# Kernel optimization log

Measured on AMD Instinct MI355X. Metric: run time of the kernel, lower is better.

The kernel has to match this reference:

```python
import jax, jax.numpy as jnp
import numpy as np

HIDDEN = 50
EPS = 1e-5


def setup_inputs() -> dict:
    key = jax.random.key(0)
    ks = jax.random.split(key, 16)
    N = 1_000_000
    G = 10_000
    xy = jax.random.normal(ks[0], (N, 2), dtype=jnp.float32)
    segment_ids = jnp.sort(jax.random.randint(ks[1], (N,), 0, G, dtype=jnp.int32))

    def lin(k, fan_in, shape):
        b = 1.0 / np.sqrt(fan_in)
        return jax.random.uniform(k, shape, jnp.float32, -b, b)

    w_init = lin(ks[2], 2, (2, HIDDEN))
    b_init = lin(ks[3], 2, (HIDDEN,))
    Ws1 = lin(ks[4], 2 * HIDDEN, (2, 2 * HIDDEN, HIDDEN))
    bs1 = lin(ks[5], 2 * HIDDEN, (2, HIDDEN))
    Ws = lin(ks[6], HIDDEN, (2, 4, HIDDEN, HIDDEN))
    bs = lin(ks[7], HIDDEN, (2, 4, HIDDEN))
    gamma = jnp.ones((2, HIDDEN), jnp.float32)
    beta = jnp.zeros((2, HIDDEN), jnp.float32)
    return {
        'xy': xy, 'segment_ids': segment_ids, 'num_graphs': G,
        'w_init': w_init, 'b_init': b_init,
        'Ws1': Ws1, 'bs1': bs1, 'Ws': Ws, 'bs': bs,
        'gamma': gamma, 'beta': beta,
    }


def reference(xy, segment_ids, num_graphs, w_init, b_init, Ws1, bs1, Ws, bs, gamma, beta):
    # node_init: [N,2] -> [N,50]
    h = xy @ w_init + b_init
    ones = jnp.ones((xy.shape[0],), h.dtype)
    counts = jax.ops.segment_sum(ones, segment_ids, num_segments=num_graphs)
    counts = jnp.maximum(counts, 1.0)[:, None]  # [G,1]
    for i in range(2):
        # dgl.mean_nodes -> per-graph mean; dgl.broadcast_nodes -> gather back
        mean = jax.ops.segment_sum(h, segment_ids, num_segments=num_graphs) / counts
        glob = mean[segment_ids]                       # [N,50]
        x = jnp.concatenate([glob, h], axis=1)         # [N,100]
        x = jax.nn.relu(x @ Ws1[i] + bs1[i])
        for j in range(3):
            x = jax.nn.relu(x @ Ws[i, j] + bs[i, j])
        x = x @ Ws[i, 3] + bs[i, 3]
        # BatchNorm1d (training mode: batch stats, biased variance)
        mu = jnp.mean(x, axis=0)
        var = jnp.mean((x - mu) ** 2, axis=0)
        h = (x - mu) * jax.lax.rsqrt(var + EPS) * gamma[i] + beta[i]
    return h
```

## Files before the change

kernel.cpp:

```cpp
#include <hip/hip_runtime.h>


#define GN 10000
#define H 50
#define EPSV 1e-5f

typedef __attribute__((ext_vector_type(4))) float f32x4;
typedef __attribute__((ext_vector_type(2))) __fp16 fp16x2;
typedef __attribute__((ext_vector_type(4))) _Float16 half4_t;

union H4 { half4_t h; uint2 u; };

static __device__ __forceinline__ f32x4 mfma16(half4_t a, half4_t b, f32x4 c){
#if __has_builtin(__builtin_amdgcn_mfma_f32_16x16x16f16)
  return __builtin_amdgcn_mfma_f32_16x16x16f16(a, b, c, 0, 0, 0);
#else
  asm volatile("v_mfma_f32_16x16x16_f16 %0, %1, %2, %0" : "+v"(c) : "v"(a), "v"(b));
  return c;
#endif
}

static __device__ __forceinline__ void split4(f32x4 v, H4& hh, H4& hl){
  fp16x2 a = __builtin_amdgcn_cvt_pkrtz(v[0], v[1]);
  fp16x2 b = __builtin_amdgcn_cvt_pkrtz(v[2], v[3]);
  hh.u.x = __builtin_bit_cast(unsigned int, a);
  hh.u.y = __builtin_bit_cast(unsigned int, b);
  float r0 = v[0] - (float)a[0];
  float r1 = v[1] - (float)a[1];
  float r2 = v[2] - (float)b[0];
  float r3 = v[3] - (float)b[1];
  fp16x2 c = __builtin_amdgcn_cvt_pkrtz(r0, r1);
  fp16x2 d = __builtin_amdgcn_cvt_pkrtz(r2, r3);
  hl.u.x = __builtin_bit_cast(unsigned int, c);
  hl.u.y = __builtin_bit_cast(unsigned int, d);
}

__global__ void k_pre(const float* __restrict__ Ws1, const float* __restrict__ Ws,
                      const float* __restrict__ bs, const int* __restrict__ sid, int N,
                      uint4* __restrict__ frag, float* __restrict__ pbias,
                      int* __restrict__ start, float* __restrict__ pzero){
  int t = blockIdx.x*blockDim.x + threadIdx.x;
  if (t < 10240){
    int lane = t & 63;
    int ks   = (t>>6) & 3;
    int Mt   = (t>>8) & 3;
    int rest = t >> 10;
    int m = rest % 5, L = rest / 5;
    const float* W = (m == 0) ? (Ws1 + L*100*H + H*H) : (Ws + (L*4 + (m-1))*H*H);
    int jo = Mt*16 + (lane & 15);
    int kb = ks*16 + ((lane>>4)<<2);
    f32x4 v;
    #pragma unroll
    for (int e = 0; e < 4; ++e){
      int k = kb + e;
      v[e] = (k < H && jo < H) ? W[k*H + jo] : 0.f;
    }
    H4 hh, hl;
    split4(v, hh, hl);
    frag[t] = make_uint4(hh.u.x, hh.u.y, hl.u.x, hl.u.y);
  } else if (t < 10752){
    int i = t - 10240;
    int j = i & 63;
    int row = i >> 6;
    pbias[i] = (j < H) ? bs[row*H + j] : 0.f;
  } else if (t < 20753){
    int g = t - 10752;
    int lo = 0, hi = N;
    while (lo < hi){ int mid = (lo+hi)>>1; if (sid[mid] < g) lo = mid+1; else hi = mid; }
    start[g] = lo;
  } else if (t >= 20800 && t < 27200){
    pzero[t - 20800] = 0.f;
  }
}

__global__ void k_ginit0(const float2* __restrict__ xy, const int* __restrict__ start,
                         const float* __restrict__ w_init, const float* __restrict__ b_init,
                         const float* __restrict__ Ws1, const float* __restrict__ bs1,
                         float* __restrict__ tg){
  __shared__ float glob[H];
  int g = blockIdx.x; int l = threadIdx.x;
  int s = start[g], e = start[g+1];
  float sx = 0.f, sy = 0.f;
  for (int n = s + l; n < e; n += 64){ float2 v = xy[n]; sx += v.x; sy += v.y; }
  #pragma unroll
  for (int off = 32; off > 0; off >>= 1){ sx += __shfl_xor(sx, off); sy += __shfl_xor(sy, off); }
  int cnt = e - s; if (cnt < 1) cnt = 1;
  float inv = 1.f/(float)cnt;
  if (l < H) glob[l] = b_init[l] + sx*inv*w_init[l] + sy*inv*w_init[H+l];
  __syncthreads();
  if (l < H){
    float a = bs1[l];
    #pragma unroll 5
    for (int k = 0; k < H; ++k) a = fmaf(glob[k], Ws1[k*H + l], a);
    tg[(size_t)g*H + l] = a;
  }
}

template<int LAYER>
__global__ __launch_bounds__(256, 3)
void k_layer(const float2* __restrict__ xy, const int* __restrict__ sid,
             const float* __restrict__ tg, const uint4* __restrict__ frag,
             const float* __restrict__ pbias,
             const float* __restrict__ w_init, const float* __restrict__ b_init,
             const float* __restrict__ stats,
             float* __restrict__ psum, float* __restrict__ psq,
             float* __restrict__ xio, int N)
{
  const int tid = threadIdx.x;
  const int wv = tid >> 6, l = tid & 63, lg = l >> 4, ll = l & 15;
  const int base = blockIdx.x*128 + wv*32;

  H4 bh[2][4], bl[2][4];
  #pragma unroll
  for (int Nt = 0; Nt < 2; ++Nt){
    int node = base + Nt*16 + ll;
    int nc = node < N ? node : N-1;
    float xv[16];
    if (LAYER == 0){
      float2 p = xy[nc];
      #pragma unroll
      for (int ks = 0; ks < 4; ++ks)
        #pragma unroll
        for (int e = 0; e < 4; ++e){
          int k = ks*16 + lg*4 + e; int kc = k < H ? k : H-1;
          xv[ks*4+e] = b_init[kc] + p.x*w_init[kc] + p.y*w_init[H+kc];
        }
    } else {
      #pragma unroll
      for (int ks = 0; ks < 4; ++ks){
        int k0 = ks*16 + lg*4;
        size_t f0 = (size_t)nc*H + k0;
        size_t fm = (size_t)N*H - 2;
        float2 u0 = *(const float2*)(xio + (f0     < fm ? f0     : fm));
        float2 u1 = *(const float2*)(xio + (f0 + 2 < fm ? f0 + 2 : fm));
        float vv[4] = {u0.x, u0.y, u1.x, u1.y};
        #pragma unroll
        for (int e = 0; e < 4; ++e){
          int kc = (k0+e) < H ? (k0+e) : H-1;
          xv[ks*4+e] = vv[e]*stats[kc] + stats[H+kc];
        }
      }
    }
    #pragma unroll
    for (int ks = 0; ks < 4; ++ks){
      f32x4 v; v[0]=xv[ks*4]; v[1]=xv[ks*4+1]; v[2]=xv[ks*4+2]; v[3]=xv[ks*4+3];
      split4(v, bh[Nt][ks], bl[Nt][ks]);
    }
  }

  f32x4 acc[4][2];
  {
    int n0 = base + ll;       n0 = n0 < N ? n0 : N-1;
    int n1 = base + 16 + ll;  n1 = n1 < N ? n1 : N-1;
    const float* t0 = tg + (size_t)sid[n0]*H;
    const float* t1 = tg + (size_t)sid[n1]*H;
    #pragma unroll
    for (int Mt = 0; Mt < 4; ++Mt)
      #pragma unroll
      for (int r = 0; r < 4; ++r){
        int j = Mt*16 + lg*4 + r; int jc = j < H ? j : H-1;
        acc[Mt][0][r] = t0[jc];
        acc[Mt][1][r] = t1[jc];
      }
  }

  #pragma unroll
  for (int m = 0; m < 5; ++m){
    const uint4* fp = frag + (LAYER*5 + m)*1024;
    #pragma unroll
    for (int Mt = 0; Mt < 4; ++Mt){
      H4 ah[4], al[4];
      #pragma unroll
      for (int ks = 0; ks < 4; ++ks){
        uint4 w = fp[(Mt*4 + ks)*64 + l];
        ah[ks].u = make_uint2(w.x, w.y);
        al[ks].u = make_uint2(w.z, w.w);
      }
      #pragma unroll
      for (int Nt = 0; Nt < 2; ++Nt){
        f32x4 c = acc[Mt][Nt];
        #pragma unroll
        for (int ks = 0; ks < 4; ++ks) c = mfma16(ah[ks].h, bh[Nt][ks].h, c);
        #pragma unroll
        for (int ks = 0; ks < 4; ++ks) c = mfma16(al[ks].h, bh[Nt][ks].h, c);
        #pragma unroll
        for (int ks = 0; ks < 4; ++ks) c = mfma16(ah[ks].h, bl[Nt][ks].h, c);
        acc[Mt][Nt] = c;
      }
    }
    if (m < 4){
      #pragma unroll
      for (int Mt = 0; Mt < 4; ++Mt){
        const f32x4 bv = *(const f32x4*)(pbias + (LAYER*4 + m)*64 + Mt*16 + (lg<<2));
        #pragma unroll
        for (int Nt = 0; Nt < 2; ++Nt){
          f32x4 v = acc[Mt][Nt];
          v[0]=fmaxf(v[0],0.f); v[1]=fmaxf(v[1],0.f); v[2]=fmaxf(v[2],0.f); v[3]=fmaxf(v[3],0.f);
          split4(v, bh[Nt][Mt], bl[Nt][Mt]);
          acc[Mt][Nt] = bv;
        }
      }
    }
  }

  #pragma unroll
  for (int Nt = 0; Nt < 2; ++Nt){
    int node = base + Nt*16 + ll;
    if (node < N){
      float* row = xio + (size_t)node*H;
      #pragma unroll
      for (int Mt = 0; Mt < 3; ++Mt){
        int j0 = Mt*16 + (lg<<2);
        *(float2*)(row + j0)     = make_float2(acc[Mt][Nt][0], acc[Mt][Nt][1]);
        *(float2*)(row + j0 + 2) = make_float2(acc[Mt][Nt][2], acc[Mt][Nt][3]);
      }
      if (lg == 0)
        *(float2*)(row + 48) = make_float2(acc[3][Nt][0], acc[3][Nt][1]);
    }
  }

  {
    int slot = (int)(blockIdx.x & 63);
    #pragma unroll
    for (int Mt = 0; Mt < 4; ++Mt)
      #pragma unroll
      for (int r = 0; r < 4; ++r){
        int j = Mt*16 + lg*4 + r;
        float s = 0.f, q = 0.f;
        #pragma unroll
        for (int Nt = 0; Nt < 2; ++Nt){
          int node = base + Nt*16 + ll;
          float v = (node < N && j < H) ? acc[Mt][Nt][r] : 0.f;
          s += v; q = fmaf(v, v, q);
        }
        #pragma unroll
        for (int off = 8; off > 0; off >>= 1){ s += __shfl_xor(s, off); q += __shfl_xor(q, off); }
        if (ll == 0 && j < H){
          atomicAdd(&psum[slot*H + j], s);
          atomicAdd(&psq [slot*H + j], q);
        }
      }
  }
}

__global__ void k_finalize(float* __restrict__ psum, float* __restrict__ psq,
                           const float* __restrict__ gamma, const float* __restrict__ beta,
                           int layer, float ninv, float* __restrict__ stats){
  int j = threadIdx.x;
  if (j >= H) return;
  float s = 0.f, q = 0.f;
  #pragma unroll 8
  for (int p = 0; p < 64; ++p){ s += psum[p*H + j]; q += psq[p*H + j]; }
  float mu  = s*ninv;
  float var = q*ninv - mu*mu;
  float a = rsqrtf(var + EPSV) * gamma[layer*H + j];
  float c = beta[layer*H + j] - mu*a;
  stats[layer*100 + j]     = a;
  stats[layer*100 + H + j] = c;
  #pragma unroll 8
  for (int p = 0; p < 64; ++p){ psum[p*H + j] = 0.f; psq[p*H + j] = 0.f; }
}

__global__ void k_gt1(const float* __restrict__ x, const int* __restrict__ start,
                      const float* __restrict__ stats,
                      const float* __restrict__ Ws1, const float* __restrict__ bs1,
                      float* __restrict__ tg){
  __shared__ float glob[H];
  int g = blockIdx.x; int j = threadIdx.x;
  int s = start[g], e = start[g+1];
  int cnt = e - s; if (cnt < 1) cnt = 1;
  float inv = 1.f/(float)cnt;
  if (j < H){
    float acc = 0.f;
    for (int n = s; n < e; ++n) acc += x[(size_t)n*H + j];
    glob[j] = acc*inv*stats[j] + stats[H+j];
  }
  __syncthreads();
  if (j < H){
    const float* W = Ws1 + 100*H;
    float a = bs1[H + j];
    #pragma unroll 5
    for (int k = 0; k < H; ++k) a = fmaf(glob[k], W[k*H + j], a);
    tg[(size_t)g*H + j] = a;
  }
}

__global__ void k_bnapply(float* __restrict__ x, const float* __restrict__ stats, int N){
  __shared__ float a[H], c[H];
  if (threadIdx.x < H){ a[threadIdx.x] = stats[100 + threadIdx.x]; c[threadIdx.x] = stats[150 + threadIdx.x]; }
  __syncthreads();
  int base = blockIdx.x * (256*H);
  int total = N*H;
  for (int idx = threadIdx.x; idx < 256*H; idx += 256){
    int i = base + idx;
    if (i < total){
      int j = idx - (idx/H)*H;
      x[i] = x[i]*a[j] + c[j];
    }
  }
}

extern "C" void kernel_launch(void* const* d_in, const int* in_sizes, int n_in,
                              void* d_out, int out_size, void* d_ws, size_t ws_size,
                              hipStream_t stream) {
  const float2* xy     = (const float2*)d_in[0];
  const int*    sid    = (const int*)d_in[1];
  const float*  w_init = (const float*)d_in[3];
  const float*  b_init = (const float*)d_in[4];
  const float*  Ws1    = (const float*)d_in[5];
  const float*  bs1    = (const float*)d_in[6];
  const float*  Ws     = (const float*)d_in[7];
  const float*  bs     = (const float*)d_in[8];
  const float*  gamma  = (const float*)d_in[9];
  const float*  beta   = (const float*)d_in[10];
  float* out = (float*)d_out;
  int N = in_sizes[0] / 2;
  const int G = GN;

  char* ws = (char*)d_ws;
  int*   start = (int*)ws;
  float* tg    = (float*)(ws + 40064);
  float* psum  = (float*)(ws + 2040064);
  float* psq   = (float*)(ws + 2052864);
  float* stats = (float*)(ws + 2065664);
  uint4* frag  = (uint4*)(ws + 2066560);
  float* pbias = (float*)(ws + 2230400);

  int nb = (N + 127)/128;

  k_pre<<<107, 256, 0, stream>>>(Ws1, Ws, bs, sid, N, frag, pbias, start, psum);
  k_ginit0<<<G, 64, 0, stream>>>(xy, start, w_init, b_init, Ws1, bs1, tg);
  k_layer<0><<<nb, 256, 0, stream>>>(xy, sid, tg, frag, pbias, w_init, b_init, stats, psum, psq, out, N);
  k_finalize<<<1, 64, 0, stream>>>(psum, psq, gamma, beta, 0, 1.0f/(float)N, stats);
  k_gt1<<<G, 64, 0, stream>>>(out, start, stats, Ws1, bs1, tg);
  k_layer<1><<<nb, 256, 0, stream>>>(xy, sid, tg, frag, pbias, w_init, b_init, stats, psum, psq, out, N);
  k_finalize<<<1, 64, 0, stream>>>(psum, psq, gamma, beta, 1, 1.0f/(float)N, stats);
  k_bnapply<<<(N + 255)/256, 256, 0, stream>>>(out, stats, N);
}
```

Baseline: 731.0 us.

## Raise layer occupancy hint, split gt1 segment sum across waves, vectorize BN apply

Three separate changes. The launch bounds hint on k_layer rises from 3 to 8 blocks per CU, which pressures the compiler to use fewer registers and may cause spilling. k_gt1 now runs 256 threads so four waves each sum a strided share of a graph's nodes, with the partial sums combined through shared memory. k_bnapply becomes a grid-stride loop over float4 elements with a modulo-based column index, cutting the number of memory instructions in the final BN pass.

```diff
diff --git a/kernel.cpp b/kernel.cpp
--- a/kernel.cpp
+++ b/kernel.cpp
@@ -97,7 +97,7 @@
 }
 
 template<int LAYER>
-__global__ __launch_bounds__(256, 3)
+__global__ __launch_bounds__(256, 8)
 void k_layer(const float2* __restrict__ xy, const int* __restrict__ sid,
              const float* __restrict__ tg, const uint4* __restrict__ frag,
              const float* __restrict__ pbias,
@@ -265,38 +265,50 @@
                       const float* __restrict__ stats,
                       const float* __restrict__ Ws1, const float* __restrict__ bs1,
                       float* __restrict__ tg){
+  __shared__ float part[4][H];
   __shared__ float glob[H];
-  int g = blockIdx.x; int j = threadIdx.x;
+  int g = blockIdx.x;
+  int t = threadIdx.x;
+  int w = t >> 6, j = t & 63;
   int s = start[g], e = start[g+1];
-  int cnt = e - s; if (cnt < 1) cnt = 1;
-  float inv = 1.f/(float)cnt;
   if (j < H){
     float acc = 0.f;
-    for (int n = s; n < e; ++n) acc += x[(size_t)n*H + j];
-    glob[j] = acc*inv*stats[j] + stats[H+j];
+    for (int n = s + w; n < e; n += 4) acc += x[(size_t)n*H + j];
+    part[w][j] = acc;
   }
   __syncthreads();
-  if (j < H){
+  if (t < H){
+    int cnt = e - s; if (cnt < 1) cnt = 1;
+    float m = (part[0][t] + part[1][t] + part[2][t] + part[3][t]) / (float)cnt;
+    glob[t] = m*stats[t] + stats[H+t];
+  }
+  __syncthreads();
+  if (t < H){
     const float* W = Ws1 + 100*H;
-    float a = bs1[H + j];
+    float a = bs1[H + t];
     #pragma unroll 5
-    for (int k = 0; k < H; ++k) a = fmaf(glob[k], W[k*H + j], a);
-    tg[(size_t)g*H + j] = a;
-  }
-}
-
-__global__ void k_bnapply(float* __restrict__ x, const float* __restrict__ stats, int N){
+    for (int k = 0; k < H; ++k) a = fmaf(glob[k], W[k*H + t], a);
+    tg[(size_t)g*H + t] = a;
+  }
+}
+
+__global__ void k_bnapply(float4* __restrict__ x4, const float* __restrict__ stats, int n4){
   __shared__ float a[H], c[H];
   if (threadIdx.x < H){ a[threadIdx.x] = stats[100 + threadIdx.x]; c[threadIdx.x] = stats[150 + threadIdx.x]; }
   __syncthreads();
-  int base = blockIdx.x * (256*H);
-  int total = N*H;
-  for (int idx = threadIdx.x; idx < 256*H; idx += 256){
-    int i = base + idx;
-    if (i < total){
-      int j = idx - (idx/H)*H;
-      x[i] = x[i]*a[j] + c[j];
-    }
+  int idx = blockIdx.x*blockDim.x + threadIdx.x;
+  int stride = gridDim.x*blockDim.x;
+  for (; idx < n4; idx += stride){
+    float4 v = x4[idx];
+    int j0 = (idx*4) % 50;
+    int j1 = j0+1; if (j1 >= 50) j1 -= 50;
+    int j2 = j0+2; if (j2 >= 50) j2 -= 50;
+    int j3 = j0+3; if (j3 >= 50) j3 -= 50;
+    v.x = v.x*a[j0] + c[j0];
+    v.y = v.y*a[j1] + c[j1];
+    v.z = v.z*a[j2] + c[j2];
+    v.w = v.w*a[j3] + c[j3];
+    x4[idx] = v;
   }
 }
 
@@ -327,13 +339,14 @@
   float* pbias = (float*)(ws + 2230400);
 
   int nb = (N + 127)/128;
+  int n4 = (N*H)/4;
 
   k_pre<<<107, 256, 0, stream>>>(Ws1, Ws, bs, sid, N, frag, pbias, start, psum);
   k_ginit0<<<G, 64, 0, stream>>>(xy, start, w_init, b_init, Ws1, bs1, tg);
   k_layer<0><<<nb, 256, 0, stream>>>(xy, sid, tg, frag, pbias, w_init, b_init, stats, psum, psq, out, N);
   k_finalize<<<1, 64, 0, stream>>>(psum, psq, gamma, beta, 0, 1.0f/(float)N, stats);
-  k_gt1<<<G, 64, 0, stream>>>(out, start, stats, Ws1, bs1, tg);
+  k_gt1<<<G, 256, 0, stream>>>(out, start, stats, Ws1, bs1, tg);
   k_layer<1><<<nb, 256, 0, stream>>>(xy, sid, tg, frag, pbias, w_init, b_init, stats, psum, psq, out, N);
   k_finalize<<<1, 64, 0, stream>>>(psum, psq, gamma, beta, 1, 1.0f/(float)N, stats);
-  k_bnapply<<<(N + 255)/256, 256, 0, stream>>>(out, stats, N);
-}
+  k_bnapply<<<4096, 256, 0, stream>>>((float4*)out, stats, n4);
+}
```

Result: slower. 1.900 ms (+159.9%).
